# Optimization experiments

Measured on AMD Instinct MI355X. Metric: run time of the kernel, lower is better.

## Reference

```python
import jax, jax.numpy as jnp
import numpy as np

B, S, D = 16, 2048, 1024
FF = 4 * D
ST, EN = 0, 512          # target_dims['start'], target_dims['end']
DT = EN - ST             # intervened subspace dim


def setup_inputs() -> dict:
    key = jax.random.key(0)
    k = jax.random.split(key, 6)
    hidden_states = jax.random.normal(k[0], (B, S, D), dtype=jnp.float32)
    eot_indices = jax.random.randint(k[1], (B,), 0, S)
    scale = 0.02
    W1 = jax.random.normal(k[2], (D, FF), dtype=jnp.float32) * scale
    W2 = jax.random.normal(k[3], (FF, D), dtype=jnp.float32) * scale
    W_rot = jax.random.normal(k[4], (DT, DT), dtype=jnp.float32) * scale
    W_inv = jax.random.normal(k[5], (DT, DT), dtype=jnp.float32) * scale
    return {"hidden_states": hidden_states, "W1": W1, "W2": W2,
            "W_rot": W_rot, "W_inv": W_inv, "eot_indices": eot_indices}


def reference(hidden_states, W1, W2, W_rot, W_inv, eot_indices):
    # layers[0]: transformer FFN block (stand-in for the wrapped encoder layer)
    h = jax.nn.gelu(hidden_states @ W1) @ W2          # [B, S, D]
    b = jnp.arange(h.shape[0])
    # LinearLayer branch: gather per-example eot row, slice target subspace
    rows = h[b, eot_indices]                          # [B, D]
    target = rows[:, ST:EN]                           # [B, DT]
    # LinearLayer -> InverseLinearLayer: rotate then un-rotate the subspace
    intervention = (target @ W_rot) @ W_inv           # [B, DT]
    # scatter/replace back into the flattened hidden states (vectorized form
    # of the per-example flatten/slice/cat/stack loop in the original code)
    new_rows = rows.at[:, ST:EN].set(intervention)    # [B, D]
    reps = h.at[b, eot_indices].set(new_rows)         # [B, S, D]
    return reps
```

## Files before the change

### kernel.cpp

```cpp
#include <hip/hip_runtime.h>
#include <hip/hip_bf16.h>
#include <stdint.h>

#define B_SZ  16
#define S_SZ  2048
#define D_SZ  1024
#define FF_SZ 4096
#define DT_SZ 512

typedef __bf16 bf16x8 __attribute__((ext_vector_type(8)));
typedef float  f32x16 __attribute__((ext_vector_type(16)));
typedef short  short8 __attribute__((ext_vector_type(8)));

__device__ __forceinline__ short f2bf(float x) {
    union { float f; uint32_t u; } v; v.f = x;
    uint32_t r = (v.u + 0x7fffu + ((v.u >> 16) & 1u)) >> 16;
    return (short)(uint16_t)r;
}

__global__ void cast_x_kernel(const float* __restrict__ src, short* __restrict__ dst, int n8) {
    int i = blockIdx.x * 256 + threadIdx.x;
    if (i >= n8) return;
    const float4* s4 = reinterpret_cast<const float4*>(src);
    float4 a = s4[2 * i], b = s4[2 * i + 1];
    short8 v;
    v[0] = f2bf(a.x); v[1] = f2bf(a.y); v[2] = f2bf(a.z); v[3] = f2bf(a.w);
    v[4] = f2bf(b.x); v[5] = f2bf(b.y); v[6] = f2bf(b.z); v[7] = f2bf(b.w);
    reinterpret_cast<short8*>(dst)[i] = v;
}

__global__ void transpose_cast_kernel(const float* __restrict__ src, short* __restrict__ dst,
                                      int R, int C) {
    __shared__ float tile[32][33];
    int c0 = blockIdx.x * 32, r0 = blockIdx.y * 32;
    int tx = threadIdx.x, ty = threadIdx.y;
#pragma unroll
    for (int i = 0; i < 32; i += 8)
        tile[ty + i][tx] = src[(size_t)(r0 + ty + i) * C + (c0 + tx)];
    __syncthreads();
#pragma unroll
    for (int i = 0; i < 32; i += 8)
        dst[(size_t)(c0 + ty + i) * R + (r0 + tx)] = f2bf(tile[tx][ty + i]);
}


#define GLOAD(srcp, dstofs)                                                   \
    __builtin_amdgcn_global_load_lds(                                         \
        (__attribute__((address_space(1))) void*)(srcp),                      \
        (__attribute__((address_space(3))) void*)(ldsb + (dstofs)), 16, 0, 0)

#define STAGE(S, T) do {                                                                    \
    _Pragma("unroll")                                                                       \
    for (int j = 0; j < 4; ++j)                                                             \
        GLOAD(gA[j] + (size_t)(T) * 64, (S) * 65536 +         j * 8192 + tid * 16);         \
    _Pragma("unroll")                                                                       \
    for (int j = 0; j < 4; ++j)                                                             \
        GLOAD(gB[j] + (size_t)(T) * 64, (S) * 65536 + 32768 + j * 8192 + tid * 16);         \
} while (0)

#define STEP(S, T, STG) do {                                                                \
    asm volatile("s_waitcnt vmcnt(0)" ::: "memory");                                        \
    __builtin_amdgcn_s_barrier();                                                           \
    if (STG) STAGE((S) ^ 1, (T) + 1);                                                       \
    __builtin_amdgcn_sched_barrier(0);                                                      \
    _Pragma("unroll")                                                                       \
    for (int ks = 0; ks < 4; ++ks) {                                                        \
        bf16x8 a[4], b[2];                                                                  \
        _Pragma("unroll")                                                                   \
        for (int mi = 0; mi < 4; ++mi)                                                      \
            a[mi] = *reinterpret_cast<const bf16x8*>(                                       \
                ldsb + (S) * 65536 + (offA0[mi] ^ (ks << 5)));                              \
        _Pragma("unroll")                                                                   \
        for (int ni = 0; ni < 2; ++ni)                                                      \
            b[ni] = *reinterpret_cast<const bf16x8*>(                                       \
                ldsb + (S) * 65536 + (offB0[ni] ^ (ks << 5)));                              \
        _Pragma("unroll")                                                                   \
        for (int mi = 0; mi < 4; ++mi)                                                      \
            _Pragma("unroll")                                                               \
            for (int ni = 0; ni < 2; ++ni)                                                  \
                acc[mi][ni] = __builtin_amdgcn_mfma_f32_32x32x16_bf16(                      \
                    a[mi], b[ni], acc[mi][ni], 0, 0, 0);                                    \
    }                                                                                       \
} while (0)

template <bool GELU_BF16>
__global__ __launch_bounds__(512, 2)
void gemm256_kernel(const short* __restrict__ A, const short* __restrict__ Bt,
                    void* __restrict__ Cout, int M, int N, int K) {
    __shared__ char lds2[2][65536];
    char* ldsb = &lds2[0][0];

    const int tid = threadIdx.x;
    const int w   = tid >> 6;
    const int l   = tid & 63;
    const int wm  = w >> 2;
    const int wn  = w & 3;
    const int l31 = l & 31;
    const int lh  = l >> 5;

    const int nwg = gridDim.x;
    int swzw = blockIdx.x;
    if ((nwg & 7) == 0) swzw = (swzw & 7) * (nwg >> 3) + (swzw >> 3);
    const int NB = N >> 8;
    const int bm = swzw / NB, bn = swzw % NB;
    const int m0 = bm << 8, n0 = bn << 8;

    int offA0[4], offB0[2];
#pragma unroll
    for (int mi = 0; mi < 4; ++mi) {
        const int r = wm * 128 + mi * 32 + l31;
        offA0[mi] = r * 128 + ((lh ^ (r & 7)) << 4);
    }
#pragma unroll
    for (int ni = 0; ni < 2; ++ni) {
        const int r = wn * 64 + ni * 32 + l31;
        offB0[ni] = 32768 + r * 128 + ((lh ^ (r & 7)) << 4);
    }

    const short *gA[4], *gB[4];
#pragma unroll
    for (int j = 0; j < 4; ++j) {
        const int X = j * 8192 + tid * 16;
        const int P = X ^ (((X >> 7) & 7) << 4);
        const int r = P >> 7, c = (P & 127) >> 1;
        gA[j] = A  + (size_t)(m0 + r) * K + c;
        gB[j] = Bt + (size_t)(n0 + r) * K + c;
    }

    f32x16 acc[4][2];
#pragma unroll
    for (int mi = 0; mi < 4; ++mi)
#pragma unroll
        for (int ni = 0; ni < 2; ++ni)
            acc[mi][ni] = (f32x16)(0.f);

    const int NT = K >> 6;

    STAGE(0, 0);

    for (int t = 0; t < NT - 2; t += 2) {
        STEP(0, t, 1);
        STEP(1, t + 1, 1);
    }
    STEP(0, NT - 2, 1);
    STEP(1, NT - 1, 0);

    const int col0 = n0 + wn * 64 + l31;
    if constexpr (GELU_BF16) {
        short* C = reinterpret_cast<short*>(Cout);
#pragma unroll
        for (int mi = 0; mi < 4; ++mi) {
            const int rb = m0 + wm * 128 + mi * 32 + 4 * lh;
#pragma unroll
            for (int ni = 0; ni < 2; ++ni)
#pragma unroll
                for (int reg = 0; reg < 16; ++reg) {
                    const int row = rb + (reg & 3) + 8 * (reg >> 2);
                    float x = acc[mi][ni][reg];
                    float u = 0.7978845608028654f * (x + 0.044715f * x * x * x);
                    float g = x / (1.f + __expf(-2.f * u));
                    C[(size_t)row * N + col0 + ni * 32] = f2bf(g);
                }
        }
    } else {
        float* C = reinterpret_cast<float*>(Cout);
#pragma unroll
        for (int mi = 0; mi < 4; ++mi) {
            const int rb = m0 + wm * 128 + mi * 32 + 4 * lh;
#pragma unroll
            for (int ni = 0; ni < 2; ++ni)
#pragma unroll
                for (int reg = 0; reg < 16; ++reg) {
                    const int row = rb + (reg & 3) + 8 * (reg >> 2);
                    C[(size_t)row * N + col0 + ni * 32] = acc[mi][ni][reg];
                }
        }
    }
}

__global__ void intervention_kernel(const float* __restrict__ Wrot, const float* __restrict__ Winv,
                                    const int* __restrict__ eot, float* __restrict__ out) {
    __shared__ float tgt[DT_SZ];
    __shared__ float tmp[DT_SZ];
    const int b = blockIdx.x;
    const int j = threadIdx.x;
    float* row = out + ((size_t)b * S_SZ + eot[b]) * D_SZ;
    tgt[j] = row[j];
    __syncthreads();
    float s = 0.f;
#pragma unroll 8
    for (int i = 0; i < DT_SZ; ++i) s = fmaf(tgt[i], Wrot[(size_t)i * DT_SZ + j], s);
    tmp[j] = s;
    __syncthreads();
    float s2 = 0.f;
#pragma unroll 8
    for (int i = 0; i < DT_SZ; ++i) s2 = fmaf(tmp[i], Winv[(size_t)i * DT_SZ + j], s2);
    row[j] = s2;
}

extern "C" void kernel_launch(void* const* d_in, const int* in_sizes, int n_in,
                              void* d_out, int out_size, void* d_ws, size_t ws_size,
                              hipStream_t stream) {
    const float* hidden = (const float*)d_in[0];
    const float* W1     = (const float*)d_in[1];
    const float* W2     = (const float*)d_in[2];
    const float* Wrot   = (const float*)d_in[3];
    const float* Winv   = (const float*)d_in[4];
    const int*   eot    = (const int*)d_in[5];
    float* out = (float*)d_out;

    const int M = B_SZ * S_SZ;

    short* W1t = (short*)d_ws;
    short* W2t = W1t + (size_t)FF_SZ * D_SZ;
    short* Xbf = W2t + (size_t)FF_SZ * D_SZ;
    const size_t fixed_bytes = 2ull * (size_t)FF_SZ * D_SZ * sizeof(short);
    const size_t per_row = (size_t)D_SZ * 2 + (size_t)FF_SZ * 2;
    size_t rem = ws_size > fixed_bytes ? ws_size - fixed_bytes : 0;
    int Mc = (int)(rem / per_row);
    Mc = (Mc / 512) * 512;
    if (Mc < 512) Mc = 512;
    if (Mc > M) Mc = M;
    short* C1 = Xbf + (size_t)Mc * D_SZ;

    transpose_cast_kernel<<<dim3(FF_SZ / 32, D_SZ / 32), dim3(32, 8), 0, stream>>>(W1, W1t, D_SZ, FF_SZ);
    transpose_cast_kernel<<<dim3(D_SZ / 32, FF_SZ / 32), dim3(32, 8), 0, stream>>>(W2, W2t, FF_SZ, D_SZ);

    for (int ms = 0; ms < M; ms += Mc) {
        const int mc = (M - ms < Mc) ? (M - ms) : Mc;
        const int n8 = mc * D_SZ / 8;
        cast_x_kernel<<<(n8 + 255) / 256, 256, 0, stream>>>(hidden + (size_t)ms * D_SZ, Xbf, n8);
        gemm256_kernel<true ><<<dim3((mc / 256) * (FF_SZ / 256)), 512, 0, stream>>>(
            Xbf, W1t, C1, mc, FF_SZ, D_SZ);
        gemm256_kernel<false><<<dim3((mc / 256) * (D_SZ / 256)), 512, 0, stream>>>(
            C1, W2t, out + (size_t)ms * D_SZ, mc, D_SZ, FF_SZ);
    }
    intervention_kernel<<<B_SZ, DT_SZ, 0, stream>>>(Wrot, Winv, eot, out);
}
```

Measured before the change: 722.5 us.

## Load GEMM B operand directly into registers, halve LDS footprint, add setprio around MFMAs

The B tile is no longer staged through LDS. Each wave loads its own B fragments straight from global memory into double-buffered registers (bA/bB), prefetching the next K step while the current one computes. This halves LDS use per block and removes the LDS reads for B. The MFMA blocks are also wrapped in s_setprio. In exchange, B is fetched redundantly across the two wm wave rows, with no LDS sharing, and register pressure rises at launch_bounds(512,2).

New measurement: 924.1 us. +27.9%, slower.

```diff
diff --git a/kernel.cpp b/kernel.cpp
--- a/kernel.cpp
+++ b/kernel.cpp
@@ -49,37 +49,37 @@
         (__attribute__((address_space(1))) void*)(srcp),                      \
         (__attribute__((address_space(3))) void*)(ldsb + (dstofs)), 16, 0, 0)
 
-#define STAGE(S, T) do {                                                                    \
-    _Pragma("unroll")                                                                       \
-    for (int j = 0; j < 4; ++j)                                                             \
-        GLOAD(gA[j] + (size_t)(T) * 64, (S) * 65536 +         j * 8192 + tid * 16);         \
-    _Pragma("unroll")                                                                       \
-    for (int j = 0; j < 4; ++j)                                                             \
-        GLOAD(gB[j] + (size_t)(T) * 64, (S) * 65536 + 32768 + j * 8192 + tid * 16);         \
-} while (0)
-
-#define STEP(S, T, STG) do {                                                                \
+#define STEP(S, BCUR, BNXT, T, STG) do {                                                    \
     asm volatile("s_waitcnt vmcnt(0)" ::: "memory");                                        \
     __builtin_amdgcn_s_barrier();                                                           \
-    if (STG) STAGE((S) ^ 1, (T) + 1);                                                       \
+    if (STG) {                                                                              \
+        _Pragma("unroll")                                                                   \
+        for (int ni = 0; ni < 2; ++ni)                                                      \
+            _Pragma("unroll")                                                               \
+            for (int ks = 0; ks < 4; ++ks)                                                  \
+                BNXT[ni * 4 + ks] = *reinterpret_cast<const bf16x8*>(                       \
+                    pB[ni] + (size_t)((T) + 1) * 64 + ks * 16);                             \
+        _Pragma("unroll")                                                                   \
+        for (int j = 0; j < 4; ++j)                                                         \
+            GLOAD(gA[j] + (size_t)((T) + 1) * 64,                                           \
+                  ((S) ^ 1) * 32768 + j * 8192 + tid * 16);                                 \
+    }                                                                                       \
     __builtin_amdgcn_sched_barrier(0);                                                      \
     _Pragma("unroll")                                                                       \
     for (int ks = 0; ks < 4; ++ks) {                                                        \
-        bf16x8 a[4], b[2];                                                                  \
+        bf16x8 a[4];                                                                        \
         _Pragma("unroll")                                                                   \
         for (int mi = 0; mi < 4; ++mi)                                                      \
             a[mi] = *reinterpret_cast<const bf16x8*>(                                       \
-                ldsb + (S) * 65536 + (offA0[mi] ^ (ks << 5)));                              \
-        _Pragma("unroll")                                                                   \
-        for (int ni = 0; ni < 2; ++ni)                                                      \
-            b[ni] = *reinterpret_cast<const bf16x8*>(                                       \
-                ldsb + (S) * 65536 + (offB0[ni] ^ (ks << 5)));                              \
+                ldsb + (S) * 32768 + (offA0[mi] ^ (ks << 5)));                              \
+        __builtin_amdgcn_s_setprio(1);                                                      \
         _Pragma("unroll")                                                                   \
         for (int mi = 0; mi < 4; ++mi)                                                      \
             _Pragma("unroll")                                                               \
             for (int ni = 0; ni < 2; ++ni)                                                  \
                 acc[mi][ni] = __builtin_amdgcn_mfma_f32_32x32x16_bf16(                      \
-                    a[mi], b[ni], acc[mi][ni], 0, 0, 0);                                    \
+                    a[mi], BCUR[ni * 4 + ks], acc[mi][ni], 0, 0, 0);                        \
+        __builtin_amdgcn_s_setprio(0);                                                      \
     }                                                                                       \
 } while (0)
 
@@ -87,7 +87,7 @@
 __global__ __launch_bounds__(512, 2)
 void gemm256_kernel(const short* __restrict__ A, const short* __restrict__ Bt,
                     void* __restrict__ Cout, int M, int N, int K) {
-    __shared__ char lds2[2][65536];
+    __shared__ char lds2[2][32768];
     char* ldsb = &lds2[0][0];
 
     const int tid = threadIdx.x;
@@ -105,27 +105,26 @@
     const int bm = swzw / NB, bn = swzw % NB;
     const int m0 = bm << 8, n0 = bn << 8;
 
-    int offA0[4], offB0[2];
+    int offA0[4];
 #pragma unroll
     for (int mi = 0; mi < 4; ++mi) {
         const int r = wm * 128 + mi * 32 + l31;
         offA0[mi] = r * 128 + ((lh ^ (r & 7)) << 4);
     }
-#pragma unroll
-    for (int ni = 0; ni < 2; ++ni) {
-        const int r = wn * 64 + ni * 32 + l31;
-        offB0[ni] = 32768 + r * 128 + ((lh ^ (r & 7)) << 4);
-    }
-
-    const short *gA[4], *gB[4];
+
+    const short* gA[4];
 #pragma unroll
     for (int j = 0; j < 4; ++j) {
         const int X = j * 8192 + tid * 16;
         const int P = X ^ (((X >> 7) & 7) << 4);
         const int r = P >> 7, c = (P & 127) >> 1;
-        gA[j] = A  + (size_t)(m0 + r) * K + c;
-        gB[j] = Bt + (size_t)(n0 + r) * K + c;
-    }
+        gA[j] = A + (size_t)(m0 + r) * K + c;
+    }
+
+    const short* pB[2];
+#pragma unroll
+    for (int ni = 0; ni < 2; ++ni)
+        pB[ni] = Bt + (size_t)(n0 + wn * 64 + ni * 32 + l31) * K + lh * 8;
 
     f32x16 acc[4][2];
 #pragma unroll
@@ -134,16 +133,24 @@
         for (int ni = 0; ni < 2; ++ni)
             acc[mi][ni] = (f32x16)(0.f);
 
+    bf16x8 bA[8], bB[8];
     const int NT = K >> 6;
 
-    STAGE(0, 0);
+#pragma unroll
+    for (int ni = 0; ni < 2; ++ni)
+#pragma unroll
+        for (int ks = 0; ks < 4; ++ks)
+            bA[ni * 4 + ks] = *reinterpret_cast<const bf16x8*>(pB[ni] + ks * 16);
+#pragma unroll
+    for (int j = 0; j < 4; ++j)
+        GLOAD(gA[j], j * 8192 + tid * 16);
 
     for (int t = 0; t < NT - 2; t += 2) {
-        STEP(0, t, 1);
-        STEP(1, t + 1, 1);
-    }
-    STEP(0, NT - 2, 1);
-    STEP(1, NT - 1, 0);
+        STEP(0, bA, bB, t, 1);
+        STEP(1, bB, bA, t + 1, 1);
+    }
+    STEP(0, bA, bB, NT - 2, 1);
+    STEP(1, bB, bA, NT - 1, 0);
 
     const int col0 = n0 + wn * 64 + l31;
     if constexpr (GELU_BF16) {
```
